# Performance work log

Measured on AMD Instinct MI355X. Metric: run time of the kernel, lower is better.

The kernel has to match this reference:

```python
import jax, jax.numpy as jnp
import numpy as np
import math

N_POINTS = 1_000_000
DIM = 3
N_LEVELS = 16
N_FEATS = 2
LOG2_HASHMAP = 19
BASE_RES = 16
DESIRED_RES = 2048
HASH_PRIMES = np.array([1, 2654435761, 805459861], dtype=np.uint32)


def _level_params():
    # faithful to original: denominator is (base_resolution - 1)
    beta = math.exp((math.log(DESIRED_RES) - math.log(BASE_RES)) / (BASE_RES - 1))
    res, hs = [], []
    for l in range(N_LEVELS):
        r = math.floor(BASE_RES * beta ** l)
        res.append(float(r))
        hs.append(min(r ** DIM, 2 ** LOG2_HASHMAP))
    return np.array(res, np.float32), np.array(hs, np.uint32)


def setup_inputs() -> dict:
    key = jax.random.key(0)
    k1, k2 = jax.random.split(key)
    x = jax.random.uniform(k1, (N_POINTS, DIM), dtype=jnp.float32)
    tables = jax.random.uniform(k2, (N_LEVELS, 2 ** LOG2_HASHMAP, N_FEATS),
                                dtype=jnp.float32, minval=-1e-4, maxval=1e-4)
    return {"x": x, "tables": tables}


def reference(x, tables):
    res_np, hs_np = _level_params()
    resolutions = jnp.asarray(res_np)           # [L]
    hashmap_sizes = jnp.asarray(hs_np)          # [L] uint32
    primes = jnp.asarray(HASH_PRIMES)           # [3] uint32
    neigs = np.arange(1 << DIM, dtype=np.int64).reshape(-1, 1)
    dims = np.arange(DIM, dtype=np.int64).reshape(1, -1)
    bin_mask = jnp.asarray((neigs & (1 << dims)) == 0)  # [8,3] bool

    def level(table, resolution, hashmap_size):
        xs = x * resolution                      # [N,3]
        xi = xs.astype(jnp.int32)                # trunc (x >= 0 so == floor)
        xf = xs - xi.astype(xs.dtype)
        xi = xi[:, None, :]                      # [N,1,3]
        xf = xf[:, None, :]
        inds = jnp.where(bin_mask, xi, xi + 1)   # [N,8,3]
        ws = jnp.where(bin_mask, 1.0 - xf, xf)   # [N,8,3]
        w = jnp.prod(ws, axis=-1, keepdims=True) # [N,8,1]
        # hash: 32-bit prime multiply, xor fold, mod hashmap_size
        h = inds.astype(jnp.uint32) * primes     # [N,8,3] (wraps mod 2^32)
        h = h[..., 0] ^ h[..., 1] ^ h[..., 2]    # [N,8]
        hid = (h % hashmap_size).astype(jnp.int32)
        return jnp.sum(table[hid] * w, axis=-2)  # [N,F]

    feats = jax.vmap(level)(tables, resolutions, hashmap_sizes)  # [L,N,F]
    feats = jnp.moveaxis(feats, 0, 1).reshape(x.shape[0], N_LEVELS * N_FEATS)
    # include_input=True
    return jnp.concatenate([x, feats], axis=-1)  # [N, 3 + L*F]
```

## Files before the change

### kernel.cpp

```cpp
#include <hip/hip_runtime.h>
#include <cstdint>
#include <cstddef>


#define NPTS     1000000
#define NLEV     16
#define TBL_ENT  524288
#define BLK      256
#define OUT_PP   35
#define CHUNKS   ((NPTS + BLK - 1) / BLK)

constexpr float    cRes[NLEV] = {16.f, 22.f, 30.f, 42.f, 58.f, 80.f, 111.f, 153.f,
                                 212.f, 294.f, 406.f, 561.f, 776.f, 1072.f, 1482.f, 2048.f};
constexpr uint32_t cHS[NLEV]  = {4096u, 10648u, 27000u, 74088u, 195112u, 512000u,
                                 524288u, 524288u, 524288u, 524288u, 524288u,
                                 524288u, 524288u, 524288u, 524288u, 524288u};


template<int L>
__device__ __forceinline__ void do_level(float px, float py, float pz,
                                         const float* __restrict__ tables,
                                         float& f0, float& f1)
{
    constexpr float    r  = cRes[L];
    constexpr uint32_t hs = cHS[L];
    const float2* __restrict__ tbl =
        reinterpret_cast<const float2*>(tables) + (size_t)L * TBL_ENT;

    const float xs = px * r, ys = py * r, zs = pz * r;
    const int xi = (int)xs, yi = (int)ys, zi = (int)zs;
    const float xf = xs - (float)xi, yf = ys - (float)yi, zf = zs - (float)zi;

    const uint32_t hx0 = (uint32_t)xi;
    const uint32_t hx1 = hx0 + 1u;
    const uint32_t hy0 = (uint32_t)yi * 2654435761u;
    const uint32_t hy1 = hy0 + 2654435761u;
    const uint32_t hz0 = (uint32_t)zi * 805459861u;
    const uint32_t hz1 = hz0 + 805459861u;

    const float wx0 = 1.f - xf, wx1 = xf;
    const float wy0 = 1.f - yf, wy1 = yf;
    const float wz0 = 1.f - zf, wz1 = zf;

    uint32_t hid[8];
    float    w[8];
    #pragma unroll
    for (int c = 0; c < 8; ++c) {
        const uint32_t hxc = (c & 1) ? hx1 : hx0;
        const uint32_t hyc = (c & 2) ? hy1 : hy0;
        const uint32_t hzc = (c & 4) ? hz1 : hz0;
        hid[c] = (hxc ^ hyc ^ hzc) % hs;
        const float wxc = (c & 1) ? wx1 : wx0;
        const float wyc = (c & 2) ? wy1 : wy0;
        const float wzc = (c & 4) ? wz1 : wz0;
        w[c] = wxc * wyc * wzc;
    }

    float2 v[8];
    #pragma unroll
    for (int c = 0; c < 8; ++c) v[c] = tbl[hid[c]];

    f0 = 0.f; f1 = 0.f;
    #pragma unroll
    for (int c = 0; c < 8; ++c) {
        f0 = fmaf(w[c], v[c].x, f0);
        f1 = fmaf(w[c], v[c].y, f1);
    }
}

__global__ __launch_bounds__(BLK) void hashgrid_pass1(
    const float* __restrict__ x,
    const float* __restrict__ tables,
    float2* __restrict__ ws)
{
    const int b = blockIdx.x;
    const int l = b / CHUNKS;
    const int c = b - l * CHUNKS;
    const int i = c * BLK + threadIdx.x;
    if (i >= NPTS) return;

    const float px = x[3 * i + 0];
    const float py = x[3 * i + 1];
    const float pz = x[3 * i + 2];

    float f0, f1;
    switch (l) {
        case 0:  do_level<0 >(px, py, pz, tables, f0, f1); break;
        case 1:  do_level<1 >(px, py, pz, tables, f0, f1); break;
        case 2:  do_level<2 >(px, py, pz, tables, f0, f1); break;
        case 3:  do_level<3 >(px, py, pz, tables, f0, f1); break;
        case 4:  do_level<4 >(px, py, pz, tables, f0, f1); break;
        case 5:  do_level<5 >(px, py, pz, tables, f0, f1); break;
        case 6:  do_level<6 >(px, py, pz, tables, f0, f1); break;
        case 7:  do_level<7 >(px, py, pz, tables, f0, f1); break;
        case 8:  do_level<8 >(px, py, pz, tables, f0, f1); break;
        case 9:  do_level<9 >(px, py, pz, tables, f0, f1); break;
        case 10: do_level<10>(px, py, pz, tables, f0, f1); break;
        case 11: do_level<11>(px, py, pz, tables, f0, f1); break;
        case 12: do_level<12>(px, py, pz, tables, f0, f1); break;
        case 13: do_level<13>(px, py, pz, tables, f0, f1); break;
        case 14: do_level<14>(px, py, pz, tables, f0, f1); break;
        default: do_level<15>(px, py, pz, tables, f0, f1); break;
    }

    ws[(size_t)l * NPTS + i] = make_float2(f0, f1);
}


__global__ __launch_bounds__(BLK) void hashgrid_pass2(
    const float* __restrict__ x,
    const float2* __restrict__ ws,
    float* __restrict__ out)
{
    __shared__ float smem[BLK * OUT_PP];

    const int t = threadIdx.x;
    const int base = blockIdx.x * BLK;
    const int i = base + t;
    const bool active = (i < NPTS);

    if (active) {
        smem[t * OUT_PP + 0] = x[3 * i + 0];
        smem[t * OUT_PP + 1] = x[3 * i + 1];
        smem[t * OUT_PP + 2] = x[3 * i + 2];
        #pragma unroll
        for (int l = 0; l < NLEV; ++l) {
            const float2 v = ws[(size_t)l * NPTS + i];
            smem[t * OUT_PP + 3 + 2 * l]     = v.x;
            smem[t * OUT_PP + 3 + 2 * l + 1] = v.y;
        }
    }
    __syncthreads();

    const size_t gbase = (size_t)blockIdx.x * (BLK * OUT_PP);
    const long long remain = (long long)NPTS * OUT_PP - (long long)gbase;
    const int n4 = (int)((remain < (long long)(BLK * OUT_PP) ? remain : (long long)(BLK * OUT_PP)) / 4);
    const float4* __restrict__ s4 = reinterpret_cast<const float4*>(smem);
    float4* __restrict__ o4 = reinterpret_cast<float4*>(out + gbase);
    for (int j = t; j < n4; j += BLK) o4[j] = s4[j];
}


__global__ __launch_bounds__(BLK) void hashgrid_fused(
    const float* __restrict__ x,
    const float* __restrict__ tables,
    float* __restrict__ out)
{
    __shared__ float smem[BLK * OUT_PP];

    const int t = threadIdx.x;
    const int i = blockIdx.x * BLK + t;
    const bool active = (i < NPTS);

    float px = 0.f, py = 0.f, pz = 0.f;
    if (active) {
        px = x[3 * i + 0];
        py = x[3 * i + 1];
        pz = x[3 * i + 2];
    }
    smem[t * OUT_PP + 0] = px;
    smem[t * OUT_PP + 1] = py;
    smem[t * OUT_PP + 2] = pz;

    float f0, f1;
    #pragma unroll
    for (int l = 0; l < NLEV; ++l) {
        switch (l) {
            case 0:  do_level<0 >(px, py, pz, tables, f0, f1); break;
            case 1:  do_level<1 >(px, py, pz, tables, f0, f1); break;
            case 2:  do_level<2 >(px, py, pz, tables, f0, f1); break;
            case 3:  do_level<3 >(px, py, pz, tables, f0, f1); break;
            case 4:  do_level<4 >(px, py, pz, tables, f0, f1); break;
            case 5:  do_level<5 >(px, py, pz, tables, f0, f1); break;
            case 6:  do_level<6 >(px, py, pz, tables, f0, f1); break;
            case 7:  do_level<7 >(px, py, pz, tables, f0, f1); break;
            case 8:  do_level<8 >(px, py, pz, tables, f0, f1); break;
            case 9:  do_level<9 >(px, py, pz, tables, f0, f1); break;
            case 10: do_level<10>(px, py, pz, tables, f0, f1); break;
            case 11: do_level<11>(px, py, pz, tables, f0, f1); break;
            case 12: do_level<12>(px, py, pz, tables, f0, f1); break;
            case 13: do_level<13>(px, py, pz, tables, f0, f1); break;
            default: do_level<15>(px, py, pz, tables, f0, f1); break;
        }
        smem[t * OUT_PP + 3 + 2 * l]     = f0;
        smem[t * OUT_PP + 3 + 2 * l + 1] = f1;
    }

    __syncthreads();

    const size_t gbase = (size_t)blockIdx.x * (BLK * OUT_PP);
    const long long remain = (long long)NPTS * OUT_PP - (long long)gbase;
    const int n4 = (int)((remain < (long long)(BLK * OUT_PP) ? remain : (long long)(BLK * OUT_PP)) / 4);
    const float4* __restrict__ s4 = reinterpret_cast<const float4*>(smem);
    float4* __restrict__ o4 = reinterpret_cast<float4*>(out + gbase);
    for (int j = t; j < n4; j += BLK) o4[j] = s4[j];
}

extern "C" void kernel_launch(void* const* d_in, const int* in_sizes, int n_in,
                              void* d_out, int out_size, void* d_ws, size_t ws_size,
                              hipStream_t stream)
{
    const float* x      = (const float*)d_in[0];
    const float* tables = (const float*)d_in[1];
    float* out          = (float*)d_out;

    const size_t ws_needed = (size_t)NLEV * NPTS * sizeof(float2);

    if (ws_size >= ws_needed) {
        float2* ws = (float2*)d_ws;
        hashgrid_pass1<<<NLEV * CHUNKS, BLK, 0, stream>>>(x, tables, ws);
        hashgrid_pass2<<<CHUNKS, BLK, 0, stream>>>(x, ws, out);
    } else {
        hashgrid_fused<<<CHUNKS, BLK, 0, stream>>>(x, tables, out);
    }
}
```

Before: 540.5 us.

## Pair adjacent hash-table gathers into float4 loads and streamline the transpose pass

Every hash table size is even. When a point's integer x coordinate is even, its two x-neighbour corners hash to adjacent entries e and e+1. The level routine therefore issues four 16-byte loads, each covering both x corners, and only reloads the x+1 corners separately for points whose x coordinate is odd. This cuts the number of scattered gather transactions, but adds lane divergence inside a wavefront where both paths run. Pass2 now processes one 64-point tile per wavefront and syncs with a waitcnt instead of a block barrier. Streaming reads and writes use nontemporal hints. The unused fused fallback also gets its missing level-14 case fixed.

```diff
diff --git a/kernel.cpp b/kernel.cpp
--- a/kernel.cpp
+++ b/kernel.cpp
@@ -9,6 +9,11 @@
 #define BLK      256
 #define OUT_PP   35
 #define CHUNKS   ((NPTS + BLK - 1) / BLK)
+#define TILES    (NPTS / 64)
+#define P2BLOCKS ((TILES + (BLK/64) - 1) / (BLK/64))
+
+typedef float f32x2 __attribute__((ext_vector_type(2)));
+typedef float f32x4 __attribute__((ext_vector_type(4)));
 
 constexpr float    cRes[NLEV] = {16.f, 22.f, 30.f, 42.f, 58.f, 80.f, 111.f, 153.f,
                                  212.f, 294.f, 406.f, 561.f, 776.f, 1072.f, 1482.f, 2048.f};
@@ -32,41 +37,54 @@
     const float xf = xs - (float)xi, yf = ys - (float)yi, zf = zs - (float)zi;
 
     const uint32_t hx0 = (uint32_t)xi;
-    const uint32_t hx1 = hx0 + 1u;
     const uint32_t hy0 = (uint32_t)yi * 2654435761u;
+    const uint32_t hz0 = (uint32_t)zi * 805459861u;
     const uint32_t hy1 = hy0 + 2654435761u;
-    const uint32_t hz0 = (uint32_t)zi * 805459861u;
     const uint32_t hz1 = hz0 + 805459861u;
+
+    const bool xodd = (xi & 1) != 0;
 
     const float wx0 = 1.f - xf, wx1 = xf;
     const float wy0 = 1.f - yf, wy1 = yf;
     const float wz0 = 1.f - zf, wz1 = zf;
 
-    uint32_t hid[8];
-    float    w[8];
+    float2 v[8];
+
+    #pragma unroll
+    for (int k = 0; k < 4; ++k) {
+        const uint32_t hyz = ((k & 1) ? hy1 : hy0) ^ ((k & 2) ? hz1 : hz0);
+        const uint32_t h0  = hx0 ^ hyz;
+        const uint32_t e   = (h0 & ~1u) % hs;
+        const float4 q = *reinterpret_cast<const float4*>(
+                             reinterpret_cast<const float*>(tbl + e));
+        const bool oh = (h0 & 1u) != 0;
+        const float2 a = make_float2(q.x, q.y);
+        const float2 b = make_float2(q.z, q.w);
+        v[2*k]   = oh ? b : a;
+        v[2*k+1] = oh ? a : b;
+    }
+
+    if (xodd) {
+        #pragma unroll
+        for (int k = 0; k < 4; ++k) {
+            const uint32_t hyz = ((k & 1) ? hy1 : hy0) ^ ((k & 2) ? hz1 : hz0);
+            const uint32_t h1  = (hx0 + 1u) ^ hyz;
+            v[2*k+1] = tbl[h1 % hs];
+        }
+    }
+
+    f0 = 0.f; f1 = 0.f;
     #pragma unroll
     for (int c = 0; c < 8; ++c) {
-        const uint32_t hxc = (c & 1) ? hx1 : hx0;
-        const uint32_t hyc = (c & 2) ? hy1 : hy0;
-        const uint32_t hzc = (c & 4) ? hz1 : hz0;
-        hid[c] = (hxc ^ hyc ^ hzc) % hs;
         const float wxc = (c & 1) ? wx1 : wx0;
         const float wyc = (c & 2) ? wy1 : wy0;
         const float wzc = (c & 4) ? wz1 : wz0;
-        w[c] = wxc * wyc * wzc;
-    }
-
-    float2 v[8];
-    #pragma unroll
-    for (int c = 0; c < 8; ++c) v[c] = tbl[hid[c]];
-
-    f0 = 0.f; f1 = 0.f;
-    #pragma unroll
-    for (int c = 0; c < 8; ++c) {
-        f0 = fmaf(w[c], v[c].x, f0);
-        f1 = fmaf(w[c], v[c].y, f1);
-    }
-}
+        const float wc  = wxc * wyc * wzc;
+        f0 = fmaf(wc, v[c].x, f0);
+        f1 = fmaf(wc, v[c].y, f1);
+    }
+}
+
 
 __global__ __launch_bounds__(BLK) void hashgrid_pass1(
     const float* __restrict__ x,
@@ -79,9 +97,9 @@
     const int i = c * BLK + threadIdx.x;
     if (i >= NPTS) return;
 
-    const float px = x[3 * i + 0];
-    const float py = x[3 * i + 1];
-    const float pz = x[3 * i + 2];
+    const float px = __builtin_nontemporal_load(&x[3 * i + 0]);
+    const float py = __builtin_nontemporal_load(&x[3 * i + 1]);
+    const float pz = __builtin_nontemporal_load(&x[3 * i + 2]);
 
     float f0, f1;
     switch (l) {
@@ -103,7 +121,9 @@
         default: do_level<15>(px, py, pz, tables, f0, f1); break;
     }
 
-    ws[(size_t)l * NPTS + i] = make_float2(f0, f1);
+    f32x2 o; o.x = f0; o.y = f1;
+    __builtin_nontemporal_store(o,
+        reinterpret_cast<f32x2*>(ws) + (size_t)l * NPTS + i);
 }
 
 
@@ -114,30 +134,33 @@
 {
     __shared__ float smem[BLK * OUT_PP];
 
-    const int t = threadIdx.x;
-    const int base = blockIdx.x * BLK;
-    const int i = base + t;
-    const bool active = (i < NPTS);
-
-    if (active) {
-        smem[t * OUT_PP + 0] = x[3 * i + 0];
-        smem[t * OUT_PP + 1] = x[3 * i + 1];
-        smem[t * OUT_PP + 2] = x[3 * i + 2];
-        #pragma unroll
-        for (int l = 0; l < NLEV; ++l) {
-            const float2 v = ws[(size_t)l * NPTS + i];
-            smem[t * OUT_PP + 3 + 2 * l]     = v.x;
-            smem[t * OUT_PP + 3 + 2 * l + 1] = v.y;
-        }
-    }
-    __syncthreads();
-
-    const size_t gbase = (size_t)blockIdx.x * (BLK * OUT_PP);
-    const long long remain = (long long)NPTS * OUT_PP - (long long)gbase;
-    const int n4 = (int)((remain < (long long)(BLK * OUT_PP) ? remain : (long long)(BLK * OUT_PP)) / 4);
-    const float4* __restrict__ s4 = reinterpret_cast<const float4*>(smem);
-    float4* __restrict__ o4 = reinterpret_cast<float4*>(out + gbase);
-    for (int j = t; j < n4; j += BLK) o4[j] = s4[j];
+    const int lane = threadIdx.x & 63;
+    const int w    = threadIdx.x >> 6;
+    const int tile = blockIdx.x * (BLK / 64) + w;
+    if (tile >= TILES) return;
+    const int i = tile * 64 + lane;
+
+    float* s = smem + w * (64 * OUT_PP);
+
+    s[lane * OUT_PP + 0] = __builtin_nontemporal_load(&x[3 * i + 0]);
+    s[lane * OUT_PP + 1] = __builtin_nontemporal_load(&x[3 * i + 1]);
+    s[lane * OUT_PP + 2] = __builtin_nontemporal_load(&x[3 * i + 2]);
+    const f32x2* __restrict__ wsv = reinterpret_cast<const f32x2*>(ws);
+    #pragma unroll
+    for (int l = 0; l < NLEV; ++l) {
+        const f32x2 v = __builtin_nontemporal_load(&wsv[(size_t)l * NPTS + i]);
+        s[lane * OUT_PP + 3 + 2 * l]     = v.x;
+        s[lane * OUT_PP + 3 + 2 * l + 1] = v.y;
+    }
+
+    asm volatile("s_waitcnt lgkmcnt(0)" ::: "memory");
+
+    const f32x4* __restrict__ s4 = reinterpret_cast<const f32x4*>(s);
+    f32x4* __restrict__ o4 =
+        reinterpret_cast<f32x4*>(out + (size_t)tile * (64 * OUT_PP));
+    #pragma unroll
+    for (int j = lane; j < (64 * OUT_PP) / 4; j += 64)
+        __builtin_nontemporal_store(s4[j], &o4[j]);
 }
 
 
@@ -180,6 +203,7 @@
             case 11: do_level<11>(px, py, pz, tables, f0, f1); break;
             case 12: do_level<12>(px, py, pz, tables, f0, f1); break;
             case 13: do_level<13>(px, py, pz, tables, f0, f1); break;
+            case 14: do_level<14>(px, py, pz, tables, f0, f1); break;
             default: do_level<15>(px, py, pz, tables, f0, f1); break;
         }
         smem[t * OUT_PP + 3 + 2 * l]     = f0;
@@ -209,7 +233,7 @@
     if (ws_size >= ws_needed) {
         float2* ws = (float2*)d_ws;
         hashgrid_pass1<<<NLEV * CHUNKS, BLK, 0, stream>>>(x, tables, ws);
-        hashgrid_pass2<<<CHUNKS, BLK, 0, stream>>>(x, ws, out);
+        hashgrid_pass2<<<P2BLOCKS, BLK, 0, stream>>>(x, ws, out);
     } else {
         hashgrid_fused<<<CHUNKS, BLK, 0, stream>>>(x, tables, out);
     }
```

Result: slower. 657.9 us (+21.7%).
